# Kernel optimization log

Measured on AMD Instinct MI355X. Metric: run time of the kernel, lower is better.

The kernel has to match this reference:

```python
import jax, jax.numpy as jnp
import numpy as np

T, B, D, H, A = 256, 512, 128, 128, 8
RUN_COUNT = 1000

def _orth(k, shape, scale):
    w = jax.random.normal(k, shape, jnp.float32)
    q, r = jnp.linalg.qr(w)
    q = q * jnp.sign(jnp.diag(r))[None, :]
    return scale * q

def setup_inputs() -> dict:
    key = jax.random.key(0)
    ks = jax.random.split(key, 12)
    return {
        'hidden': jnp.zeros((B, H), jnp.float32),
        'obs': jax.random.normal(ks[0], (T, B, D), jnp.float32),
        'dones': (jax.random.randint(ks[1], (T, B), 0, 10) == 0),
        'mean_obs': jax.random.normal(ks[2], (D,), jnp.float32) * 0.1,
        'welford_S': jax.random.uniform(ks[3], (D,), jnp.float32) * RUN_COUNT,
        'running_count': RUN_COUNT,
        'W_emb': _orth(ks[4], (D, H), float(np.sqrt(2.0))), 'b_emb': jnp.zeros((H,), jnp.float32),
        'Wi': jax.random.normal(ks[5], (H, 3 * H), jnp.float32) / np.sqrt(H),
        'Wh': jax.random.normal(ks[6], (H, 3 * H), jnp.float32) / np.sqrt(H),
        'bh': jnp.zeros((3 * H,), jnp.float32),
        'W_act': _orth(ks[7], (H, H), 2.0), 'b_act': jnp.zeros((H,), jnp.float32),
        'W_alpha': _orth(ks[8], (H, A), 0.01), 'b_alpha': jnp.zeros((A,), jnp.float32),
        'W_beta': _orth(ks[9], (H, A), 0.01), 'b_beta': jnp.zeros((A,), jnp.float32),
    }

def _welford(M0, S0, count0, xs):
    # sequential Welford update over stacked rows, as in the original lax.scan
    def step(carry, x):
        M, S, c = carry
        c = c + 1.0
        M_new = M + (x - M) / c
        S_new = S + (x - M) * (x - M_new)
        return (M_new, S_new, c), None
    (M, S, c), _ = jax.lax.scan(step, (M0, S0, jnp.asarray(count0, jnp.float32)), xs)
    return M, S, c

def reference(hidden, obs, dones, mean_obs, welford_S, running_count,
              W_emb, b_emb, Wi, Wh, bh, W_act, b_act, W_alpha, b_alpha, W_beta, b_beta):
    # --- running-stat normalization (running_count > 0 branch) ---
    stacked = obs.reshape(-1, obs.shape[-1])  # [T*B, D]
    M, S, c = _welford(mean_obs, welford_S, running_count, stacked)
    var = S / (c - 1.0)
    obs_n = (obs - M) / (jnp.sqrt(var) + 1e-8)
    # --- embedding MLP ---
    emb = jax.nn.relu(obs_n @ W_emb + b_emb)  # [T, B, H]
    # --- GRU scan over time; precompute input-side gate projections (no input bias, flax GRUCell) ---
    xg = emb @ Wi  # [T, B, 3H]
    def gru_step(h, inp):
        x3, reset = inp
        h = jnp.where(reset[:, None], 0.0, h)  # reset carry where done
        hg = h @ Wh + bh
        xr, xz, xn = jnp.split(x3, 3, axis=-1)
        hr, hz, hn = jnp.split(hg, 3, axis=-1)
        r = jax.nn.sigmoid(xr + hr)
        z = jax.nn.sigmoid(xz + hz)
        n = jnp.tanh(xn + r * hn)
        h_new = (1.0 - z) * n + z * h
        return h_new, h_new
    h_last, ys = jax.lax.scan(gru_step, hidden, (xg, dones))  # ys: [T, B, H]
    # --- policy heads ---
    act = jax.nn.relu(ys @ W_act + b_act)
    alpha = jax.nn.softplus(act @ W_alpha + b_alpha) + 1.0
    beta = jax.nn.softplus(act @ W_beta + b_beta) + 1.0
    return h_last, alpha, beta, M, S
```

## Files before the change

### kernel.cpp

```cpp
#include <hip/hip_runtime.h>

#define T_DIM 256
#define B_DIM 512
#define D_DIM 128
#define H_DIM 128
#define A_DIM 8
#define N_ROWS (T_DIM*B_DIM)
#define NT (N_ROWS/16)
#define NWIN 8

typedef __attribute__((ext_vector_type(4))) float f32x4;
typedef __attribute__((ext_vector_type(8))) short bf16x8;
typedef __attribute__((ext_vector_type(4))) short bf16x4;
typedef __attribute__((ext_vector_type(8))) _Float16 f16x8;
typedef __attribute__((ext_vector_type(4))) unsigned u32x4;

#define OFF_PSUM   0ull
#define OFF_PSQ    1048576ull
#define OFF_STATM  2097152ull
#define OFF_STATI  2097664ull
#define OFF_WEMB   2098176ull
#define OFF_WI     2130944ull
#define OFF_WH     2229248ull
#define OFF_WACT   2425856ull
#define OFF_WHEAD  2458624ull
#define OFF_TLO    2462720ull
#define OFF_UH     2463744ull
#define OFF_XG     4194304ull
#define OFF_YS     104857600ull

#define OUT_H      0
#define OUT_ALPHA  65536
#define OUT_BETA   1114112
#define OUT_M      2162688
#define OUT_S      2162816

__device__ inline short f2bf(float x){
  union { float f; unsigned u; } v; v.f = x;
  unsigned r = v.u + 0x7FFFu + ((v.u>>16)&1u);
  return (short)(r>>16);
}
__device__ inline float bf2f(short h){
  union { unsigned u; float f; } v; v.u = ((unsigned)(unsigned short)h)<<16; return v.f;
}

__global__ __launch_bounds__(256) void k_partial(const float* __restrict__ obs,
                                                 double* __restrict__ psum,
                                                 double* __restrict__ psq){
  int tid = threadIdx.x; int col = tid & 127; int rh = tid >> 7;
  double s = 0.0, q = 0.0;
  for (int r = blockIdx.x*2 + rh; r < N_ROWS; r += 2048){
    float v = obs[(size_t)r*D_DIM + col];
    s += (double)v; q += (double)v*(double)v;
  }
  __shared__ double ls[256], lq[256];
  ls[tid]=s; lq[tid]=q; __syncthreads();
  if (rh==0){
    psum[(size_t)blockIdx.x*128 + col] = ls[tid] + ls[tid+128];
    psq [(size_t)blockIdx.x*128 + col] = lq[tid] + lq[tid+128];
  }
}

__global__ __launch_bounds__(1024) void k_stats(const double* __restrict__ psum,
                                                const double* __restrict__ psq,
                                                const float* __restrict__ mean_obs,
                                                const float* __restrict__ welfS,
                                                const int* __restrict__ runcnt,
                                                float* __restrict__ outM, float* __restrict__ outS,
                                                float* __restrict__ wsM,  float* __restrict__ wsI){
  int tid = threadIdx.x; int col = tid & 127; int seg = tid >> 7;
  double s=0.0, q=0.0;
  for (int b=seg; b<1024; b+=8){ s += psum[(size_t)b*128+col]; q += psq[(size_t)b*128+col]; }
  __shared__ double ls[1024], lq[1024];
  ls[tid]=s; lq[tid]=q; __syncthreads();
  if (seg==0){
    for (int b=1;b<8;b++){ s += ls[b*128+col]; q += lq[b*128+col]; }
    double c0 = (double)runcnt[0];
    double Nn = (double)N_ROWS;
    double n  = c0 + Nn;
    double M0 = (double)mean_obs[col], S0 = (double)welfS[col];
    double mb = s / Nn;
    double delta = mb - M0;
    double M = M0 + delta * Nn / n;
    double M2b = q - Nn*mb*mb;
    double S = S0 + M2b + delta*delta*c0*Nn/n;
    double var = S / (n - 1.0);
    float inv = (float)(1.0/(sqrt(var)+1e-8));
    outM[col] = (float)M; outS[col] = (float)S;
    wsM[col]  = (float)M; wsI[col]  = inv;
  }
}

__global__ void k_pack_all(const float* __restrict__ W_emb, const float* __restrict__ Wi,
                           const float* __restrict__ Wh,    const float* __restrict__ W_act,
                           const float* __restrict__ W_al,  const float* __restrict__ W_be,
                           short* __restrict__ Bemb, short* __restrict__ BWi,
                           short* __restrict__ BWh,  short* __restrict__ Bact,
                           short* __restrict__ Bhead){
  int gidx = blockIdx.x*256 + threadIdx.x;
  if (gidx >= 133120) return;
  if (gidx >= 131072){
    int idx = gidx - 131072;
    int j = idx & 7, lane = (idx>>3)&63, kb = (idx>>9)&3;
    int k = kb*32 + (lane>>4)*8 + j;
    int n = lane & 15;
    float wv = (n<8) ? W_al[(size_t)k*8 + n] : W_be[(size_t)k*8 + (n-8)];
    Bhead[idx] = f2bf(wv);
    return;
  }
  const float* src; short* dst; int C; int fmt; int idx;
  if (gidx < 16384)      { src=W_emb; dst=Bemb; C=128; fmt=0; idx=gidx; }
  else if (gidx < 65536) { src=Wi;    dst=BWi;  C=384; fmt=0; idx=gidx-16384; }
  else if (gidx < 114688){ src=Wh;    dst=BWh;  C=384; fmt=1; idx=gidx-65536; }
  else                   { src=W_act; dst=Bact; C=128; fmt=0; idx=gidx-114688; }
  int j = idx & 7, lane = (idx>>3)&63, kb = (idx>>9)&3, ct = idx>>11;
  int k = kb*32 + (lane>>4)*8 + j;
  int n = ct*16 + (lane&15);
  float wv = src[(size_t)k*C + n];
  short h;
  if (fmt==0) h = f2bf(wv);
  else { union { _Float16 hf; short s; } u; u.hf = (_Float16)wv; h = u.s; }
  dst[idx] = h;
}

__global__ __launch_bounds__(512) void k_sched(const unsigned char* __restrict__ dones,
                                               int* __restrict__ tlo,
                                               unsigned char* __restrict__ usehid){
  int k = blockIdx.x;
  int b = threadIdx.x;
  int t0 = 0, uh = 1;
  if (k > 0){
    for (int t = 32*k; t >= 0; t--){
      if (dones[(size_t)t*B_DIM + b]){ t0 = t; uh = 0; break; }
    }
  }
  usehid[k*B_DIM + b] = (unsigned char)uh;
  __shared__ int red[512];
  red[b] = t0; __syncthreads();
  if (b < 32){
    int m = red[b*16];
    #pragma unroll
    for (int i=1;i<16;i++) m = min(m, red[b*16+i]);
    tlo[k*32 + b] = m;
  }
}

__global__ __launch_bounds__(512) void k_embxg(const float* __restrict__ obs,
                                               const float* __restrict__ wsM,
                                               const float* __restrict__ wsI,
                                               const short* __restrict__ Bemb,
                                               const float* __restrict__ b_emb,
                                               const short* __restrict__ BWi,
                                               short* __restrict__ xgpk){
  int tid=threadIdx.x, w=tid>>6, lane=tid&63, q=lane>>4, l=lane&15;
  int rt = blockIdx.x;
  int r0 = rt*16;
  __shared__ __align__(16) short obsL[16][136];
  __shared__ __align__(16) short embL[16][136];

  {
    int row = tid>>5, seg = tid&31;
    f32x4 o = *(const f32x4*)(obs + (size_t)(r0+row)*D_DIM + seg*4);
    f32x4 m = *(const f32x4*)(wsM + seg*4);
    f32x4 iv= *(const f32x4*)(wsI + seg*4);
    bf16x4 v;
    v[0]=f2bf((o[0]-m[0])*iv[0]); v[1]=f2bf((o[1]-m[1])*iv[1]);
    v[2]=f2bf((o[2]-m[2])*iv[2]); v[3]=f2bf((o[3]-m[3])*iv[3]);
    *(bf16x4*)&obsL[row][seg*4] = v;
  }
  __syncthreads();

  bf16x8 A[4];
  #pragma unroll
  for (int kb=0;kb<4;kb++) A[kb] = *(const bf16x8*)&obsL[l][kb*32+q*8];

  const bf16x8* BE = (const bf16x8*)Bemb;
  f32x4 accE = {0.f,0.f,0.f,0.f};
  #pragma unroll
  for (int kb=0;kb<4;kb++)
    accE = __builtin_amdgcn_mfma_f32_16x16x32_bf16(A[kb], BE[(w*4+kb)*64+lane], accE, 0,0,0);
  {
    float bb = b_emb[w*16 + l];
    #pragma unroll
    for (int r2=0;r2<4;r2++){
      float e = accE[r2] + bb; e = e>0.f ? e : 0.f;
      embL[q*4+r2][w*16+l] = f2bf(e);
    }
  }
  __syncthreads();

  bf16x8 A2[4];
  #pragma unroll
  for (int kb=0;kb<4;kb++) A2[kb] = *(const bf16x8*)&embL[l][kb*32+q*8];

  const bf16x8* BW = (const bf16x8*)BWi;
  bf16x4* xg4 = (bf16x4*)xgpk;
  #pragma unroll
  for (int g=0; g<3; g++){
    int ct = g*8 + w;
    f32x4 acc = {0.f,0.f,0.f,0.f};
    #pragma unroll
    for (int kb=0;kb<4;kb++)
      acc = __builtin_amdgcn_mfma_f32_16x16x32_bf16(A2[kb], BW[(ct*4+kb)*64+lane], acc, 0,0,0);
    bf16x4 v;
    v[0]=f2bf(acc[0]); v[1]=f2bf(acc[1]); v[2]=f2bf(acc[2]); v[3]=f2bf(acc[3]);
    xg4[((size_t)rt*24 + ct)*64 + lane] = v;
  }
}

#define LDB(g,kb) __builtin_bit_cast(f16x8, pw4[(((g)*8+w)*4+(kb))*64+lane])
__global__
__attribute__((amdgpu_flat_work_group_size(512,512)))
__attribute__((amdgpu_waves_per_eu(2,2)))
void k_gru(const float* __restrict__ hidden,
           const unsigned char* __restrict__ dones,
           const short* __restrict__ xgpk,
           const short* __restrict__ BWh,
           const float* __restrict__ bh,
           const int* __restrict__ tlo,
           const unsigned char* __restrict__ usehid,
           short* __restrict__ yspk,
           float* __restrict__ h_last){
  int tid=threadIdx.x, w=tid>>6, lane=tid&63, q=lane>>4, l=lane&15;
  int kk = blockIdx.x >> 5, bt = blockIdx.x & 31;
  int t_out0 = kk*32;
  int t_end  = t_out0 + 32;
  int t_start = tlo[kk*32 + bt];

  __shared__ __align__(16) _Float16 hF[2][16][136];

  const u32x4* pw4 = (const u32x4*)BWh;
  f16x8 B00 = LDB(0,0), B01 = LDB(0,1), B02 = LDB(0,2), B03 = LDB(0,3);
  f16x8 B10 = LDB(1,0), B11 = LDB(1,1), B12 = LDB(1,2), B13 = LDB(1,3);
  f16x8 B20 = LDB(2,0), B21 = LDB(2,1), B22 = LDB(2,2), B23 = LDB(2,3);

  float bh0 = bh[0*128 + w*16 + l];
  float bh1 = bh[1*128 + w*16 + l];
  float bh2 = bh[2*128 + w*16 + l];

  float hv[4];
  #pragma unroll
  for (int r2=0;r2<4;r2++){
    int b = bt*16 + q*4 + r2;
    hv[r2] = usehid[kk*B_DIM + b] ? hidden[(size_t)b*H_DIM + w*16 + l] : 0.f;
  }

  const bf16x4* xgt = (const bf16x4*)xgpk + (((size_t)t_start*32 + bt)*24 + w)*64 + lane;
  const unsigned char* dnp = dones + (size_t)t_start*B_DIM + bt*16 + q*4;
  bf16x4* yst = (bf16x4*)yspk + (((size_t)t_start*32 + bt)*8 + w)*64 + lane;

  bf16x4 xr_c = xgt[0], xz_c = xgt[512], xn_c = xgt[1024];
  unsigned dn_c = *(const unsigned*)dnp;

  for (int t = t_start; t < t_end; t++){
    int buf = t & 1;
    #pragma unroll
    for (int r2=0;r2<4;r2++){
      float hvv = ((dn_c >> (r2*8)) & 255u) ? 0.f : hv[r2];
      hv[r2] = hvv;
      hF[buf][q*4+r2][w*16+l] = (_Float16)hvv;
    }
    __syncthreads();

    int adv = (t+1 < t_end) ? 1 : 0;
    xgt += (size_t)adv * 49152;
    dnp += adv * B_DIM;
    bf16x4 xr_n = xgt[0], xz_n = xgt[512], xn_n = xgt[1024];
    unsigned dn_n = *(const unsigned*)dnp;

    f16x8 A0 = *(const f16x8*)&hF[buf][l][0*32+q*8];
    f16x8 A1 = *(const f16x8*)&hF[buf][l][1*32+q*8];
    f16x8 A2 = *(const f16x8*)&hF[buf][l][2*32+q*8];
    f16x8 A3 = *(const f16x8*)&hF[buf][l][3*32+q*8];

    f32x4 acc0 = {0.f,0.f,0.f,0.f}, acc1 = {0.f,0.f,0.f,0.f}, acc2 = {0.f,0.f,0.f,0.f};
    acc0 = __builtin_amdgcn_mfma_f32_16x16x32_f16(A0, B00, acc0, 0,0,0);
    acc1 = __builtin_amdgcn_mfma_f32_16x16x32_f16(A0, B10, acc1, 0,0,0);
    acc2 = __builtin_amdgcn_mfma_f32_16x16x32_f16(A0, B20, acc2, 0,0,0);
    acc0 = __builtin_amdgcn_mfma_f32_16x16x32_f16(A1, B01, acc0, 0,0,0);
    acc1 = __builtin_amdgcn_mfma_f32_16x16x32_f16(A1, B11, acc1, 0,0,0);
    acc2 = __builtin_amdgcn_mfma_f32_16x16x32_f16(A1, B21, acc2, 0,0,0);
    acc0 = __builtin_amdgcn_mfma_f32_16x16x32_f16(A2, B02, acc0, 0,0,0);
    acc1 = __builtin_amdgcn_mfma_f32_16x16x32_f16(A2, B12, acc1, 0,0,0);
    acc2 = __builtin_amdgcn_mfma_f32_16x16x32_f16(A2, B22, acc2, 0,0,0);
    acc0 = __builtin_amdgcn_mfma_f32_16x16x32_f16(A3, B03, acc0, 0,0,0);
    acc1 = __builtin_amdgcn_mfma_f32_16x16x32_f16(A3, B13, acc1, 0,0,0);
    acc2 = __builtin_amdgcn_mfma_f32_16x16x32_f16(A3, B23, acc2, 0,0,0);

    #pragma unroll
    for (int r2=0;r2<4;r2++){
      float xr = bf2f(xr_c[r2]), xz = bf2f(xz_c[r2]), xn = bf2f(xn_c[r2]);
      float rg = 1.f/(1.f + __expf(-(xr + acc0[r2] + bh0)));
      float zg = 1.f/(1.f + __expf(-(xz + acc1[r2] + bh1)));
      float nu = xn + rg*(acc2[r2] + bh2);
      float e2 = __expf(2.f*nu);
      float ng = 1.f - 2.f/(e2 + 1.f);
      hv[r2] = (1.f - zg)*ng + zg*hv[r2];
    }
    if (t >= t_out0){
      bf16x4 yv;
      yv[0]=f2bf(hv[0]); yv[1]=f2bf(hv[1]); yv[2]=f2bf(hv[2]); yv[3]=f2bf(hv[3]);
      *yst = yv;
    }
    yst += 16384;
    xr_c = xr_n; xz_c = xz_n; xn_c = xn_n; dn_c = dn_n;
  }

  if (kk == NWIN-1){
    #pragma unroll
    for (int r2=0;r2<4;r2++)
      h_last[(size_t)(bt*16+q*4+r2)*H_DIM + w*16 + l] = hv[r2];
  }
}

__global__ __launch_bounds__(256) void k_heads(const short* __restrict__ yspk,
                                               const short* __restrict__ Bact,
                                               const float* __restrict__ b_act,
                                               const short* __restrict__ Bhead,
                                               const float* __restrict__ b_alpha,
                                               const float* __restrict__ b_beta,
                                               float* __restrict__ alpha,
                                               float* __restrict__ beta){
  int tid=threadIdx.x, w=tid>>6, lane=tid&63, q=lane>>4, l=lane&15;
  size_t rt = (size_t)blockIdx.x*4 + w;
  __shared__ __align__(16) short tl[4][16][136];
  const bf16x4* ys4 = (const bf16x4*)yspk;
  #pragma unroll
  for (int ct=0; ct<8; ct++){
    bf16x4 v = ys4[(rt*8+ct)*64+lane];
    #pragma unroll
    for (int r2=0;r2<4;r2++) tl[w][q*4+r2][ct*16+l] = v[r2];
  }
  __syncthreads();
  bf16x8 A[4];
  #pragma unroll
  for (int kb=0;kb<4;kb++) A[kb] = *(const bf16x8*)&tl[w][l][kb*32+q*8];
  __syncthreads();
  const bf16x8* BA = (const bf16x8*)Bact;
  f32x4 accA[8];
  #pragma unroll
  for (int ct=0;ct<8;ct++){ f32x4 z = {0.f,0.f,0.f,0.f}; accA[ct]=z; }
  #pragma unroll
  for (int ct=0;ct<8;ct++)
    #pragma unroll
    for (int kb=0;kb<4;kb++)
      accA[ct] = __builtin_amdgcn_mfma_f32_16x16x32_bf16(A[kb], BA[(ct*4+kb)*64+lane], accA[ct], 0,0,0);
  #pragma unroll
  for (int ct=0;ct<8;ct++){
    int col = ct*16 + l;
    float bb = b_act[col];
    #pragma unroll
    for (int r2=0;r2<4;r2++){
      float e = accA[ct][r2] + bb; e = e>0.f ? e : 0.f;
      tl[w][q*4+r2][col] = f2bf(e);
    }
  }
  __syncthreads();
  bf16x8 A2[4];
  #pragma unroll
  for (int kb=0;kb<4;kb++) A2[kb] = *(const bf16x8*)&tl[w][l][kb*32+q*8];
  const bf16x8* BHd = (const bf16x8*)Bhead;
  f32x4 acc = {0.f,0.f,0.f,0.f};
  #pragma unroll
  for (int kb=0;kb<4;kb++)
    acc = __builtin_amdgcn_mfma_f32_16x16x32_bf16(A2[kb], BHd[kb*64+lane], acc, 0,0,0);
  float bb = (l<8) ? b_alpha[l] : b_beta[l-8];
  float* dst = (l<8) ? alpha : beta;
  int cc = (l<8) ? l : l-8;
  #pragma unroll
  for (int r2=0;r2<4;r2++){
    float u = acc[r2] + bb;
    float sp = fmaxf(u,0.f) + log1pf(expf(-fabsf(u)));
    dst[(rt*16 + q*4 + r2)*8 + cc] = sp + 1.f;
  }
}

extern "C" void kernel_launch(void* const* d_in, const int* in_sizes, int n_in,
                              void* d_out, int out_size, void* d_ws, size_t ws_size,
                              hipStream_t stream){
  const float* hidden   = (const float*)d_in[0];
  const float* obs      = (const float*)d_in[1];
  const unsigned char* dones = (const unsigned char*)d_in[2];
  const float* mean_obs = (const float*)d_in[3];
  const float* welfS    = (const float*)d_in[4];
  const int*   runcnt   = (const int*)d_in[5];
  const float* W_emb = (const float*)d_in[6];
  const float* b_emb = (const float*)d_in[7];
  const float* Wi    = (const float*)d_in[8];
  const float* Wh    = (const float*)d_in[9];
  const float* bh    = (const float*)d_in[10];
  const float* W_act = (const float*)d_in[11];
  const float* b_act = (const float*)d_in[12];
  const float* W_al  = (const float*)d_in[13];
  const float* b_al  = (const float*)d_in[14];
  const float* W_be  = (const float*)d_in[15];
  const float* b_be  = (const float*)d_in[16];
  float* out = (float*)d_out;
  char*  ws  = (char*)d_ws;

  double* psum = (double*)(ws + OFF_PSUM);
  double* psq  = (double*)(ws + OFF_PSQ);
  float*  wsM  = (float*)(ws + OFF_STATM);
  float*  wsI  = (float*)(ws + OFF_STATI);
  short*  Bemb = (short*)(ws + OFF_WEMB);
  short*  BWi  = (short*)(ws + OFF_WI);
  short*  BWh  = (short*)(ws + OFF_WH);
  short*  Bact = (short*)(ws + OFF_WACT);
  short*  Bhead= (short*)(ws + OFF_WHEAD);
  int*    tlo  = (int*)(ws + OFF_TLO);
  unsigned char* uh = (unsigned char*)(ws + OFF_UH);
  short*  xgpk = (short*)(ws + OFF_XG);
  short*  yspk = (short*)(ws + OFF_YS);

  k_partial<<<1024,256,0,stream>>>(obs, psum, psq);
  k_stats<<<1,1024,0,stream>>>(psum, psq, mean_obs, welfS, runcnt,
                               out+OUT_M, out+OUT_S, wsM, wsI);
  k_sched<<<8,512,0,stream>>>(dones, tlo, uh);
  k_pack_all<<<520,256,0,stream>>>(W_emb, Wi, Wh, W_act, W_al, W_be,
                                   Bemb, BWi, BWh, Bact, Bhead);
  k_embxg<<<8192,512,0,stream>>>(obs, wsM, wsI, Bemb, b_emb, BWi, xgpk);
  k_gru<<<256,512,0,stream>>>(hidden, dones, xgpk, BWh, bh, tlo, uh,
                              yspk, out + OUT_H);
  k_heads<<<2048,256,0,stream>>>(yspk, Bact, b_act, Bhead, b_al, b_be,
                                 out + OUT_ALPHA, out + OUT_BETA);
}
```

Before: 623.4 us.

## Prescale GRU gates by log2e, fold biases into xg, swizzle LDS, use fast intrinsics

```diff
diff --git a/kernel.cpp b/kernel.cpp
--- a/kernel.cpp
+++ b/kernel.cpp
@@ -8,6 +8,7 @@
 #define N_ROWS (T_DIM*B_DIM)
 #define NT (N_ROWS/16)
 #define NWIN 8
+#define LOG2E 1.4426950408889634f
 
 typedef __attribute__((ext_vector_type(4))) float f32x4;
 typedef __attribute__((ext_vector_type(8))) short bf16x8;
@@ -43,6 +44,8 @@
 __device__ inline float bf2f(short h){
   union { unsigned u; float f; } v; v.u = ((unsigned)(unsigned short)h)<<16; return v.f;
 }
+
+__device__ inline int swz(int row, int col){ return row*136 + (col ^ ((row&7)<<3)); }
 
 __global__ __launch_bounds__(256) void k_partial(const float* __restrict__ obs,
                                                  double* __restrict__ psum,
@@ -119,7 +122,10 @@
   float wv = src[(size_t)k*C + n];
   short h;
   if (fmt==0) h = f2bf(wv);
-  else { union { _Float16 hf; short s; } u; u.hf = (_Float16)wv; h = u.s; }
+  else {
+    wv *= (n < 256) ? LOG2E : (2.f*LOG2E);
+    union { _Float16 hf; short s; } u; u.hf = (_Float16)wv; h = u.s;
+  }
   dst[idx] = h;
 }
 
@@ -151,12 +157,13 @@
                                                const short* __restrict__ Bemb,
                                                const float* __restrict__ b_emb,
                                                const short* __restrict__ BWi,
+                                               const float* __restrict__ bh,
                                                short* __restrict__ xgpk){
   int tid=threadIdx.x, w=tid>>6, lane=tid&63, q=lane>>4, l=lane&15;
   int rt = blockIdx.x;
   int r0 = rt*16;
-  __shared__ __align__(16) short obsL[16][136];
-  __shared__ __align__(16) short embL[16][136];
+  __shared__ __align__(16) short obsL[16*136];
+  __shared__ __align__(16) short embL[16*136];
 
   {
     int row = tid>>5, seg = tid&31;
@@ -166,13 +173,13 @@
     bf16x4 v;
     v[0]=f2bf((o[0]-m[0])*iv[0]); v[1]=f2bf((o[1]-m[1])*iv[1]);
     v[2]=f2bf((o[2]-m[2])*iv[2]); v[3]=f2bf((o[3]-m[3])*iv[3]);
-    *(bf16x4*)&obsL[row][seg*4] = v;
+    *(bf16x4*)&obsL[swz(row, seg*4)] = v;
   }
   __syncthreads();
 
   bf16x8 A[4];
   #pragma unroll
-  for (int kb=0;kb<4;kb++) A[kb] = *(const bf16x8*)&obsL[l][kb*32+q*8];
+  for (int kb=0;kb<4;kb++) A[kb] = *(const bf16x8*)&obsL[swz(l, kb*32+q*8)];
 
   const bf16x8* BE = (const bf16x8*)Bemb;
   f32x4 accE = {0.f,0.f,0.f,0.f};
@@ -184,14 +191,15 @@
     #pragma unroll
     for (int r2=0;r2<4;r2++){
       float e = accE[r2] + bb; e = e>0.f ? e : 0.f;
-      embL[q*4+r2][w*16+l] = f2bf(e);
+      int b = q*4+r2;
+      embL[swz(b, w*16+l)] = f2bf(e);
     }
   }
   __syncthreads();
 
   bf16x8 A2[4];
   #pragma unroll
-  for (int kb=0;kb<4;kb++) A2[kb] = *(const bf16x8*)&embL[l][kb*32+q*8];
+  for (int kb=0;kb<4;kb++) A2[kb] = *(const bf16x8*)&embL[swz(l, kb*32+q*8)];
 
   const bf16x8* BW = (const bf16x8*)BWi;
   bf16x4* xg4 = (bf16x4*)xgpk;
@@ -202,8 +210,12 @@
     #pragma unroll
     for (int kb=0;kb<4;kb++)
       acc = __builtin_amdgcn_mfma_f32_16x16x32_bf16(A2[kb], BW[(ct*4+kb)*64+lane], acc, 0,0,0);
+    int col = ct*16 + l;
+    float bb = (g<2) ? bh[col] : 0.f;
+    float sc = (g<2) ? LOG2E : (2.f*LOG2E);
     bf16x4 v;
-    v[0]=f2bf(acc[0]); v[1]=f2bf(acc[1]); v[2]=f2bf(acc[2]); v[3]=f2bf(acc[3]);
+    v[0]=f2bf((acc[0]+bb)*sc); v[1]=f2bf((acc[1]+bb)*sc);
+    v[2]=f2bf((acc[2]+bb)*sc); v[3]=f2bf((acc[3]+bb)*sc);
     xg4[((size_t)rt*24 + ct)*64 + lane] = v;
   }
 }
@@ -227,16 +239,14 @@
   int t_end  = t_out0 + 32;
   int t_start = tlo[kk*32 + bt];
 
-  __shared__ __align__(16) _Float16 hF[2][16][136];
+  __shared__ __align__(16) _Float16 hF[2][16*136];
 
   const u32x4* pw4 = (const u32x4*)BWh;
   f16x8 B00 = LDB(0,0), B01 = LDB(0,1), B02 = LDB(0,2), B03 = LDB(0,3);
   f16x8 B10 = LDB(1,0), B11 = LDB(1,1), B12 = LDB(1,2), B13 = LDB(1,3);
   f16x8 B20 = LDB(2,0), B21 = LDB(2,1), B22 = LDB(2,2), B23 = LDB(2,3);
 
-  float bh0 = bh[0*128 + w*16 + l];
-  float bh1 = bh[1*128 + w*16 + l];
-  float bh2 = bh[2*128 + w*16 + l];
+  float bh2c = bh[2*128 + w*16 + l] * (2.f*LOG2E);
 
   float hv[4];
   #pragma unroll
@@ -258,9 +268,12 @@
     for (int r2=0;r2<4;r2++){
       float hvv = ((dn_c >> (r2*8)) & 255u) ? 0.f : hv[r2];
       hv[r2] = hvv;
-      hF[buf][q*4+r2][w*16+l] = (_Float16)hvv;
-    }
-    __syncthreads();
+      int b = q*4+r2;
+      hF[buf][swz(b, w*16+l)] = (_Float16)hvv;
+    }
+    asm volatile("s_waitcnt lgkmcnt(0)" ::: "memory");
+    __builtin_amdgcn_s_barrier();
+    asm volatile("" ::: "memory");
 
     int adv = (t+1 < t_end) ? 1 : 0;
     xgt += (size_t)adv * 49152;
@@ -268,10 +281,11 @@
     bf16x4 xr_n = xgt[0], xz_n = xgt[512], xn_n = xgt[1024];
     unsigned dn_n = *(const unsigned*)dnp;
 
-    f16x8 A0 = *(const f16x8*)&hF[buf][l][0*32+q*8];
-    f16x8 A1 = *(const f16x8*)&hF[buf][l][1*32+q*8];
-    f16x8 A2 = *(const f16x8*)&hF[buf][l][2*32+q*8];
-    f16x8 A3 = *(const f16x8*)&hF[buf][l][3*32+q*8];
+    const _Float16* hb = &hF[buf][0];
+    f16x8 A0 = *(const f16x8*)(hb + swz(l,  0 + q*8));
+    f16x8 A1 = *(const f16x8*)(hb + swz(l, 32 + q*8));
+    f16x8 A2 = *(const f16x8*)(hb + swz(l, 64 + q*8));
+    f16x8 A3 = *(const f16x8*)(hb + swz(l, 96 + q*8));
 
     f32x4 acc0 = {0.f,0.f,0.f,0.f}, acc1 = {0.f,0.f,0.f,0.f}, acc2 = {0.f,0.f,0.f,0.f};
     acc0 = __builtin_amdgcn_mfma_f32_16x16x32_f16(A0, B00, acc0, 0,0,0);
@@ -290,12 +304,11 @@
     #pragma unroll
     for (int r2=0;r2<4;r2++){
       float xr = bf2f(xr_c[r2]), xz = bf2f(xz_c[r2]), xn = bf2f(xn_c[r2]);
-      float rg = 1.f/(1.f + __expf(-(xr + acc0[r2] + bh0)));
-      float zg = 1.f/(1.f + __expf(-(xz + acc1[r2] + bh1)));
-      float nu = xn + rg*(acc2[r2] + bh2);
-      float e2 = __expf(2.f*nu);
-      float ng = 1.f - 2.f/(e2 + 1.f);
-      hv[r2] = (1.f - zg)*ng + zg*hv[r2];
+      float rg = __builtin_amdgcn_rcpf(1.f + __builtin_amdgcn_exp2f(-(xr + acc0[r2])));
+      float zg = __builtin_amdgcn_rcpf(1.f + __builtin_amdgcn_exp2f(-(xz + acc1[r2])));
+      float e2 = __builtin_amdgcn_exp2f(xn + rg*(acc2[r2] + bh2c));
+      float ng = 1.f - 2.f*__builtin_amdgcn_rcpf(e2 + 1.f);
+      hv[r2] = ng + zg*(hv[r2] - ng);
     }
     if (t >= t_out0){
       bf16x4 yv;
@@ -323,18 +336,18 @@
                                                float* __restrict__ beta){
   int tid=threadIdx.x, w=tid>>6, lane=tid&63, q=lane>>4, l=lane&15;
   size_t rt = (size_t)blockIdx.x*4 + w;
-  __shared__ __align__(16) short tl[4][16][136];
+  __shared__ __align__(16) short tl[4][16*136];
   const bf16x4* ys4 = (const bf16x4*)yspk;
   #pragma unroll
   for (int ct=0; ct<8; ct++){
     bf16x4 v = ys4[(rt*8+ct)*64+lane];
     #pragma unroll
-    for (int r2=0;r2<4;r2++) tl[w][q*4+r2][ct*16+l] = v[r2];
+    for (int r2=0;r2<4;r2++){ int b=q*4+r2; tl[w][swz(b, ct*16+l)] = v[r2]; }
   }
   __syncthreads();
   bf16x8 A[4];
   #pragma unroll
-  for (int kb=0;kb<4;kb++) A[kb] = *(const bf16x8*)&tl[w][l][kb*32+q*8];
+  for (int kb=0;kb<4;kb++) A[kb] = *(const bf16x8*)&tl[w][swz(l, kb*32+q*8)];
   __syncthreads();
   const bf16x8* BA = (const bf16x8*)Bact;
   f32x4 accA[8];
@@ -352,13 +365,14 @@
     #pragma unroll
     for (int r2=0;r2<4;r2++){
       float e = accA[ct][r2] + bb; e = e>0.f ? e : 0.f;
-      tl[w][q*4+r2][col] = f2bf(e);
+      int b = q*4+r2;
+      tl[w][swz(b, col)] = f2bf(e);
     }
   }
   __syncthreads();
   bf16x8 A2[4];
   #pragma unroll
-  for (int kb=0;kb<4;kb++) A2[kb] = *(const bf16x8*)&tl[w][l][kb*32+q*8];
+  for (int kb=0;kb<4;kb++) A2[kb] = *(const bf16x8*)&tl[w][swz(l, kb*32+q*8)];
   const bf16x8* BHd = (const bf16x8*)Bhead;
   f32x4 acc = {0.f,0.f,0.f,0.f};
   #pragma unroll
@@ -370,7 +384,8 @@
   #pragma unroll
   for (int r2=0;r2<4;r2++){
     float u = acc[r2] + bb;
-    float sp = fmaxf(u,0.f) + log1pf(expf(-fabsf(u)));
+    float e = __builtin_amdgcn_exp2f(-fabsf(u)*LOG2E);
+    float sp = fmaxf(u,0.f) + 0.6931471805599453f*__builtin_amdgcn_logf(1.f + e);
     dst[(rt*16 + q*4 + r2)*8 + cc] = sp + 1.f;
   }
 }
@@ -418,7 +433,7 @@
   k_sched<<<8,512,0,stream>>>(dones, tlo, uh);
   k_pack_all<<<520,256,0,stream>>>(W_emb, Wi, Wh, W_act, W_al, W_be,
                                    Bemb, BWi, BWh, Bact, Bhead);
-  k_embxg<<<8192,512,0,stream>>>(obs, wsM, wsI, Bemb, b_emb, BWi, xgpk);
+  k_embxg<<<8192,512,0,stream>>>(obs, wsM, wsI, Bemb, b_emb, BWi, bh, xgpk);
   k_gru<<<256,512,0,stream>>>(hidden, dones, xgpk, BWh, bh, tlo, uh,
                               yspk, out + OUT_H);
   k_heads<<<2048,256,0,stream>>>(yspk, Bact, b_act, Bhead, b_al, b_be,
```

New measurement: 509.5 us. -18.3%, faster.
